# Performance work log

Hardware: AMD Instinct MI355X
Metric: run time of the kernel (lower is better)

Reference implementation:

```python
import jax, jax.numpy as jnp
import numpy as np

EPS = 1e-6      # torch F.pairwise_distance default eps (added to the difference)
MARGIN = 0.5


def setup_inputs() -> dict:
    key = jax.random.key(0)
    k1, k2 = jax.random.split(key)
    batch = jax.random.normal(k1, (8192, 1024), dtype=jnp.float32)
    positive = jax.random.normal(k2, (1024,), dtype=jnp.float32)
    return {"batch": batch, "positive": positive}


def _loss(batch, positive):
    n, d = batch.shape
    # torch pairwise_distance(x, y) = ||x - y + eps||_2, so
    # ||a - b + eps||^2 = ||a||^2 + ||b||^2 - 2 a.b + 2*eps*(sum(a) - sum(b)) + d*eps^2
    sq = jnp.sum(batch * batch, axis=-1)                 # [n]
    dots = batch @ batch.T                               # [n, n] GEMM
    sums = jnp.sum(batch, axis=-1)                       # [n]
    d2 = (sq[:, None] + sq[None, :] - 2.0 * dots
          + 2.0 * EPS * (sums[:, None] - sums[None, :]) + d * EPS * EPS)
    # exclude self (the python loop concatenates batch[:i], batch[i+1:])
    neg_inf = jnp.asarray(-jnp.inf, d2.dtype)
    d2_masked = jnp.where(jnp.eye(n, dtype=bool), neg_inf, d2)
    max_neg = jnp.sqrt(jnp.maximum(jnp.max(d2_masked, axis=-1), 0.0))  # [n]
    # distance anchor -> positive (with torch eps convention)
    diff = batch - positive[None, :] + EPS
    pos_dist = jnp.sqrt(jnp.sum(diff * diff, axis=-1))   # [n]
    losses = jax.nn.relu(pos_dist - max_neg + MARGIN)    # [n]
    # anchors exactly equal to the positive are skipped in the original loop
    valid = ~jnp.all(batch == positive[None, :], axis=-1)
    cnt = jnp.sum(valid.astype(losses.dtype))
    return jnp.sum(jnp.where(valid, losses, 0.0)) / cnt


def reference(batch, positive):
    return _loss(batch, positive)
```

## Files before the change

### kernel.cpp

```cpp
#include <hip/hip_runtime.h>
#include <hip/hip_bf16.h>


#define NROWS 8192
#define DIM   1024
#define BTM   256
#define BTN   128
#define BK    32
#define NKT   (DIM / BK)
#define NUNITS 1056

constexpr float EPS = 1e-6f;
constexpr float MARGIN = 0.5f;

typedef __attribute__((ext_vector_type(8))) short short8;
typedef __attribute__((ext_vector_type(4))) float f32x4;

__device__ __forceinline__ unsigned short f2bf_rne(float f) {
    unsigned u = __float_as_uint(f);
    u += 0x7fffu + ((u >> 16) & 1u);
    return (unsigned short)(u >> 16);
}

__global__ void prep_kernel(const float* __restrict__ X, const float* __restrict__ P,
                            unsigned short* __restrict__ Xb,
                            float* __restrict__ cj, float* __restrict__ basei,
                            float* __restrict__ posd, int* __restrict__ valid)
{
    const int tid  = threadIdx.x;
    const int w    = tid >> 6;
    const int lane = tid & 63;
    const int row  = blockIdx.x * 4 + w;
    const float* xr = X + (size_t)row * DIM;

    float sq = 0.f, sm = 0.f, pd = 0.f;
    bool eq = true;
    #pragma unroll
    for (int it = 0; it < 4; ++it) {
        const int idx = it * 256 + lane * 4;
        const float4 x = *(const float4*)(xr + idx);
        const float4 p = *(const float4*)(P + idx);
        sq += x.x*x.x + x.y*x.y + x.z*x.z + x.w*x.w;
        sm += x.x + x.y + x.z + x.w;
        const float d0 = x.x - p.x + EPS, d1 = x.y - p.y + EPS;
        const float d2 = x.z - p.z + EPS, d3 = x.w - p.w + EPS;
        pd += d0*d0 + d1*d1 + d2*d2 + d3*d3;
        eq = eq && (x.x == p.x) && (x.y == p.y) && (x.z == p.z) && (x.w == p.w);
        ushort4 b;
        b.x = f2bf_rne(x.x); b.y = f2bf_rne(x.y); b.z = f2bf_rne(x.z); b.w = f2bf_rne(x.w);
        *(ushort4*)(Xb + (size_t)row * DIM + idx) = b;
    }
    #pragma unroll
    for (int off = 32; off >= 1; off >>= 1) {
        sq += __shfl_xor(sq, off);
        sm += __shfl_xor(sm, off);
        pd += __shfl_xor(pd, off);
    }
    const bool alleq = __all(eq);
    if (lane == 0) {
        cj[row]    = sq - 2.f * EPS * sm;
        basei[row] = sq + 2.f * EPS * sm + (float)DIM * EPS * EPS;
        posd[row]  = sqrtf(pd);
        valid[row] = alleq ? 0 : 1;
    }
}

__global__ __launch_bounds__(512, 4) void gemm_max_kernel(
        const unsigned short* __restrict__ Xb,
        const float* __restrict__ cj,
        float* __restrict__ partmax)
{
    __shared__ alignas(16) unsigned short lds[3][1536 * 8];

    const int tid  = threadIdx.x;
    const int lane = tid & 63;
    const int wid  = tid >> 6;
    const int wm   = wid >> 1;
    const int wn   = wid & 1;
    const int l15  = lane & 15;
    const int lk   = lane >> 4;
    const int cx   = lk ^ ((l15 >> 1) & 3);

    {
        const unsigned h = ((unsigned)blockIdx.x * 2654435761u) >> 29;
        for (unsigned i = 0; i < h; ++i) __builtin_amdgcn_s_sleep(2);
    }

    const int t0 = (blockIdx.x & 7) * (NUNITS / 8) + (blockIdx.x >> 3);
    int bm = (int)(32.5f - sqrtf(1056.25f - (float)t0));
    if (bm < 0) bm = 0;
    if (bm > 31) bm = 31;
    while (bm > 0 && 65 * bm - bm * bm > t0) --bm;
    while (65 * (bm + 1) - (bm + 1) * (bm + 1) <= t0) ++bm;
    const int bn = 2 * bm + (t0 - (65 * bm - bm * bm));
    const int Mbase = bm * BTM, Nbase = bn * BTN;

    f32x4 acc[4][4];
    #pragma unroll
    for (int m = 0; m < 4; ++m)
        #pragma unroll
        for (int n = 0; n < 4; ++n)
            acc[m][n] = (f32x4){0.f, 0.f, 0.f, 0.f};

    const int qa0 = tid,        ra0 = qa0 >> 2, ca0 = (qa0 & 3) ^ ((qa0 >> 3) & 3);
    const int qa1 = 512 + tid,  ra1 = qa1 >> 2, ca1 = (qa1 & 3) ^ ((qa1 >> 3) & 3);
    const unsigned short* sA0 = Xb + (size_t)(Mbase + ra0) * DIM + ca0 * 8;
    const unsigned short* sA1 = Xb + (size_t)(Mbase + ra1) * DIM + ca1 * 8;
    const unsigned short* sB0 = Xb + (size_t)(Nbase + ra0) * DIM + ca0 * 8;

    #define STAGE_K(SB, KT) do {                                                              \
        __builtin_amdgcn_global_load_lds((const __attribute__((address_space(1))) void*)(sA0 + (KT) * BK), \
                (__attribute__((address_space(3))) void*)(&lds[SB][(wid * 64) * 8]), 16, 0, 0); \
        __builtin_amdgcn_global_load_lds((const __attribute__((address_space(1))) void*)(sA1 + (KT) * BK), \
                (__attribute__((address_space(3))) void*)(&lds[SB][(512 + wid * 64) * 8]), 16, 0, 0); \
        __builtin_amdgcn_global_load_lds((const __attribute__((address_space(1))) void*)(sB0 + (KT) * BK), \
                (__attribute__((address_space(3))) void*)(&lds[SB][(1024 + wid * 64) * 8]), 16, 0, 0); \
    } while (0)

    const int aoff = ((wm * 64 + l15) * 4 + cx) * 8;
    const int boff = 1024 * 8 + ((wn * 64 + l15) * 4 + cx) * 8;

    #define KT_BODY(RB, SB, KTS, VMC, DOSTAGE) do {                                           \
        asm volatile("s_waitcnt vmcnt(" #VMC ")" ::: "memory");                               \
        __builtin_amdgcn_s_barrier();                                                         \
        __builtin_amdgcn_sched_barrier(0);                                                    \
        if (DOSTAGE) STAGE_K(SB, KTS);                                                        \
        short8 af[4], bf[4];                                                                  \
        _Pragma("unroll")                                                                     \
        for (int mt = 0; mt < 4; ++mt)                                                        \
            af[mt] = *(const short8*)(&lds[RB][0] + aoff + mt * 512);                         \
        _Pragma("unroll")                                                                     \
        for (int nt = 0; nt < 4; ++nt)                                                        \
            bf[nt] = *(const short8*)(&lds[RB][0] + boff + nt * 512);                         \
        __builtin_amdgcn_s_setprio(1);                                                        \
        _Pragma("unroll")                                                                     \
        for (int mt = 0; mt < 4; ++mt)                                                        \
            _Pragma("unroll")                                                                 \
            for (int nt = 0; nt < 4; ++nt)                                                    \
                acc[mt][nt] = __builtin_amdgcn_mfma_f32_16x16x32_bf16(af[mt], bf[nt], acc[mt][nt], 0, 0, 0); \
        __builtin_amdgcn_s_setprio(0);                                                        \
    } while (0)

    STAGE_K(0, 0);
    STAGE_K(1, 1);

    for (int ktb = 0; ktb < 30; ktb += 3) {
        KT_BODY(0, 2, ktb + 2, 3, true);
        KT_BODY(1, 0, ktb + 3, 3, true);
        KT_BODY(2, 1, ktb + 4, 3, true);
    }
    KT_BODY(0, 2, 0, 3, false);
    KT_BODY(1, 2, 0, 0, false);
    #undef KT_BODY
    #undef STAGE_K

    float* scratchf = (float*)&lds[0][0];
    float cv[4];
    #pragma unroll
    for (int n = 0; n < 4; ++n)
        cv[n] = cj[Nbase + wn * 64 + n * 16 + l15];

    float vt[4];
    #pragma unroll
    for (int n = 0; n < 4; ++n) vt[n] = -__builtin_inff();

    #pragma unroll
    for (int m = 0; m < 4; ++m) {
        #pragma unroll
        for (int r = 0; r < 4; ++r) {
            const int lrow = wm * 64 + m * 16 + lk * 4 + r;
            const int grow = Mbase + lrow;
            const float ci = cj[grow];
            float rv = -__builtin_inff();
            #pragma unroll
            for (int n = 0; n < 4; ++n) {
                const float dot2 = 2.f * acc[m][n][r];
                const bool dg = (grow == Nbase + wn * 64 + n * 16 + l15);
                float vr = cv[n] - dot2;
                float vc = ci - dot2;
                if (dg) { vr = -__builtin_inff(); vc = -__builtin_inff(); }
                rv = fmaxf(rv, vr);
                vt[n] = fmaxf(vt[n], vc);
            }
            #pragma unroll
            for (int off = 8; off >= 1; off >>= 1)
                rv = fmaxf(rv, __shfl_xor(rv, off));
            if (l15 == 0) scratchf[wn * 256 + lrow] = rv;
        }
    }
    #pragma unroll
    for (int n = 0; n < 4; ++n) {
        vt[n] = fmaxf(vt[n], __shfl_xor(vt[n], 16));
        vt[n] = fmaxf(vt[n], __shfl_xor(vt[n], 32));
        if (lk == 0) scratchf[512 + wm * 128 + wn * 64 + n * 16 + l15] = vt[n];
    }
    __syncthreads();

    if (tid < BTM) {
        partmax[(size_t)bn * NROWS + Mbase + tid] = fmaxf(scratchf[tid], scratchf[256 + tid]);
    } else if (tid < BTM + BTN) {
        const int c = tid - BTM;
        const float v = fmaxf(fmaxf(scratchf[512 + c], scratchf[640 + c]),
                              fmaxf(scratchf[768 + c], scratchf[896 + c]));
        partmax[(size_t)(64 + bm) * NROWS + Nbase + c] = v;
    }
}

__global__ void finalize1_kernel(const float* __restrict__ partmax,
                                 const float* __restrict__ basei,
                                 const float* __restrict__ posd,
                                 const int* __restrict__ valid,
                                 float* __restrict__ partials)
{
    const int tid = threadIdx.x;
    const int a   = blockIdx.x;
    const int row = a * 256 + tid;
    float m = -__builtin_inff();
    for (int bn = 2 * a; bn < 64; ++bn)
        m = fmaxf(m, partmax[(size_t)bn * NROWS + row]);
    for (int bm2 = 0; bm2 <= a; ++bm2)
        m = fmaxf(m, partmax[(size_t)(64 + bm2) * NROWS + row]);
    const float d2 = m + basei[row];
    const float mn = sqrtf(fmaxf(d2, 0.f));
    float loss = fmaxf(posd[row] - mn + MARGIN, 0.f);
    float cnt = 1.f;
    if (!valid[row]) { loss = 0.f; cnt = 0.f; }
    #pragma unroll
    for (int off = 32; off >= 1; off >>= 1) {
        loss += __shfl_xor(loss, off);
        cnt  += __shfl_xor(cnt, off);
    }
    __shared__ float sl[4], sc[4];
    const int w = tid >> 6, lane = tid & 63;
    if (lane == 0) { sl[w] = loss; sc[w] = cnt; }
    __syncthreads();
    if (tid == 0) {
        partials[blockIdx.x * 2]     = sl[0] + sl[1] + sl[2] + sl[3];
        partials[blockIdx.x * 2 + 1] = sc[0] + sc[1] + sc[2] + sc[3];
    }
}

__global__ void finalize2_kernel(const float* __restrict__ partials, float* __restrict__ out)
{
    const int tid = threadIdx.x;
    float l = 0.f, c = 0.f;
    if (tid < 32) { l = partials[tid * 2]; c = partials[tid * 2 + 1]; }
    #pragma unroll
    for (int off = 32; off >= 1; off >>= 1) {
        l += __shfl_xor(l, off);
        c += __shfl_xor(c, off);
    }
    if (tid == 0) out[0] = l / c;
}

extern "C" void kernel_launch(void* const* d_in, const int* in_sizes, int n_in,
                              void* d_out, int out_size, void* d_ws, size_t ws_size,
                              hipStream_t stream)
{
    const float* X = (const float*)d_in[0];
    const float* P = (const float*)d_in[1];
    float* out = (float*)d_out;
    char* ws = (char*)d_ws;

    unsigned short* Xb = (unsigned short*)ws;
    size_t off = (size_t)NROWS * DIM * sizeof(unsigned short);
    float* cj    = (float*)(ws + off);  off += (size_t)NROWS * 4;
    float* basei = (float*)(ws + off);  off += (size_t)NROWS * 4;
    float* posd  = (float*)(ws + off);  off += (size_t)NROWS * 4;
    int*   valid = (int*)(ws + off);    off += (size_t)NROWS * 4;
    float* partmax = (float*)(ws + off); off += (size_t)96 * NROWS * 4;
    float* partials = (float*)(ws + off);

    prep_kernel<<<NROWS / 4, 256, 0, stream>>>(X, P, Xb, cj, basei, posd, valid);
    gemm_max_kernel<<<NUNITS, 512, 0, stream>>>(Xb, cj, partmax);
    finalize1_kernel<<<NROWS / 256, 256, 0, stream>>>(partmax, basei, posd, valid, partials);
    finalize2_kernel<<<1, 64, 0, stream>>>(partials, out);
}
```

Baseline: 112.9 us.

## Fuse row-max reduction and loss finalize into GEMM via atomics and last-block

Replaces the per-tile partial-max buffer and two finalize kernels with order-preserving unsigned atomicMax into a per-row max array. A global counter marks the last-finishing GEMM block, which then computes the loss and mean directly. This removes two kernel launches and the write and read of the large partial-max buffer. In exchange it adds contention on the row-max atomics and leaves the final reduction serialized in a single block.

```diff
diff --git a/kernel.cpp b/kernel.cpp
--- a/kernel.cpp
+++ b/kernel.cpp
@@ -22,16 +22,27 @@
     return (unsigned short)(u >> 16);
 }
 
+__device__ __forceinline__ unsigned fkey(float f) {
+    unsigned b = __float_as_uint(f);
+    return (b & 0x80000000u) ? ~b : (b | 0x80000000u);
+}
+__device__ __forceinline__ float finv(unsigned k) {
+    return __uint_as_float((k & 0x80000000u) ? (k & 0x7FFFFFFFu) : ~k);
+}
+
 __global__ void prep_kernel(const float* __restrict__ X, const float* __restrict__ P,
                             unsigned short* __restrict__ Xb,
                             float* __restrict__ cj, float* __restrict__ basei,
-                            float* __restrict__ posd, int* __restrict__ valid)
+                            float* __restrict__ posd, int* __restrict__ valid,
+                            unsigned* __restrict__ rowmax_u, unsigned* __restrict__ counter)
 {
     const int tid  = threadIdx.x;
     const int w    = tid >> 6;
     const int lane = tid & 63;
     const int row  = blockIdx.x * 4 + w;
     const float* xr = X + (size_t)row * DIM;
+
+    if (blockIdx.x == 0 && tid == 0) *counter = 0u;
 
     float sq = 0.f, sm = 0.f, pd = 0.f;
     bool eq = true;
@@ -58,19 +69,27 @@
     }
     const bool alleq = __all(eq);
     if (lane == 0) {
-        cj[row]    = sq - 2.f * EPS * sm;
-        basei[row] = sq + 2.f * EPS * sm + (float)DIM * EPS * EPS;
-        posd[row]  = sqrtf(pd);
-        valid[row] = alleq ? 0 : 1;
+        cj[row]       = sq - 2.f * EPS * sm;
+        basei[row]    = sq + 2.f * EPS * sm + (float)DIM * EPS * EPS;
+        posd[row]     = sqrtf(pd);
+        valid[row]    = alleq ? 0 : 1;
+        rowmax_u[row] = 0u;
     }
 }
 
 __global__ __launch_bounds__(512, 4) void gemm_max_kernel(
         const unsigned short* __restrict__ Xb,
         const float* __restrict__ cj,
-        float* __restrict__ partmax)
+        const float* __restrict__ basei,
+        const float* __restrict__ posd,
+        const int* __restrict__ valid,
+        unsigned* __restrict__ rowmax_u,
+        unsigned* __restrict__ counter,
+        float* __restrict__ out)
 {
     __shared__ alignas(16) unsigned short lds[3][1536 * 8];
+    __shared__ int lastflag;
+    __shared__ float sl[8], sc[8];
 
     const int tid  = threadIdx.x;
     const int lane = tid & 63;
@@ -197,60 +216,47 @@
     __syncthreads();
 
     if (tid < BTM) {
-        partmax[(size_t)bn * NROWS + Mbase + tid] = fmaxf(scratchf[tid], scratchf[256 + tid]);
+        const float v = fmaxf(scratchf[tid], scratchf[256 + tid]);
+        atomicMax(&rowmax_u[Mbase + tid], fkey(v));
     } else if (tid < BTM + BTN) {
         const int c = tid - BTM;
         const float v = fmaxf(fmaxf(scratchf[512 + c], scratchf[640 + c]),
                               fmaxf(scratchf[768 + c], scratchf[896 + c]));
-        partmax[(size_t)(64 + bm) * NROWS + Nbase + c] = v;
-    }
-}
-
-__global__ void finalize1_kernel(const float* __restrict__ partmax,
-                                 const float* __restrict__ basei,
-                                 const float* __restrict__ posd,
-                                 const int* __restrict__ valid,
-                                 float* __restrict__ partials)
-{
-    const int tid = threadIdx.x;
-    const int a   = blockIdx.x;
-    const int row = a * 256 + tid;
-    float m = -__builtin_inff();
-    for (int bn = 2 * a; bn < 64; ++bn)
-        m = fmaxf(m, partmax[(size_t)bn * NROWS + row]);
-    for (int bm2 = 0; bm2 <= a; ++bm2)
-        m = fmaxf(m, partmax[(size_t)(64 + bm2) * NROWS + row]);
-    const float d2 = m + basei[row];
-    const float mn = sqrtf(fmaxf(d2, 0.f));
-    float loss = fmaxf(posd[row] - mn + MARGIN, 0.f);
-    float cnt = 1.f;
-    if (!valid[row]) { loss = 0.f; cnt = 0.f; }
+        atomicMax(&rowmax_u[Nbase + c], fkey(v));
+    }
+
+    __threadfence();
+    __syncthreads();
+    if (tid == 0) {
+        const unsigned old = atomicAdd(counter, 1u);
+        lastflag = (old == NUNITS - 1) ? 1 : 0;
+    }
+    __syncthreads();
+    if (!lastflag) return;
+    __threadfence();
+
+    float lsum = 0.f, csum = 0.f;
+    for (int r = tid; r < NROWS; r += 512) {
+        const unsigned k = atomicMax(&rowmax_u[r], 0u);
+        const float m = finv(k);
+        const float d2 = m + basei[r];
+        const float mn = sqrtf(fmaxf(d2, 0.f));
+        const float loss = fmaxf(posd[r] - mn + MARGIN, 0.f);
+        if (valid[r]) { lsum += loss; csum += 1.f; }
+    }
     #pragma unroll
     for (int off = 32; off >= 1; off >>= 1) {
-        loss += __shfl_xor(loss, off);
-        cnt  += __shfl_xor(cnt, off);
-    }
-    __shared__ float sl[4], sc[4];
-    const int w = tid >> 6, lane = tid & 63;
-    if (lane == 0) { sl[w] = loss; sc[w] = cnt; }
+        lsum += __shfl_xor(lsum, off);
+        csum += __shfl_xor(csum, off);
+    }
+    if (lane == 0) { sl[wid] = lsum; sc[wid] = csum; }
     __syncthreads();
     if (tid == 0) {
-        partials[blockIdx.x * 2]     = sl[0] + sl[1] + sl[2] + sl[3];
-        partials[blockIdx.x * 2 + 1] = sc[0] + sc[1] + sc[2] + sc[3];
-    }
-}
-
-__global__ void finalize2_kernel(const float* __restrict__ partials, float* __restrict__ out)
-{
-    const int tid = threadIdx.x;
-    float l = 0.f, c = 0.f;
-    if (tid < 32) { l = partials[tid * 2]; c = partials[tid * 2 + 1]; }
-    #pragma unroll
-    for (int off = 32; off >= 1; off >>= 1) {
-        l += __shfl_xor(l, off);
-        c += __shfl_xor(c, off);
-    }
-    if (tid == 0) out[0] = l / c;
+        float L = 0.f, C = 0.f;
+        #pragma unroll
+        for (int i = 0; i < 8; ++i) { L += sl[i]; C += sc[i]; }
+        out[0] = L / C;
+    }
 }
 
 extern "C" void kernel_launch(void* const* d_in, const int* in_sizes, int n_in,
@@ -268,11 +274,11 @@
     float* basei = (float*)(ws + off);  off += (size_t)NROWS * 4;
     float* posd  = (float*)(ws + off);  off += (size_t)NROWS * 4;
     int*   valid = (int*)(ws + off);    off += (size_t)NROWS * 4;
-    float* partmax = (float*)(ws + off); off += (size_t)96 * NROWS * 4;
-    float* partials = (float*)(ws + off);
-
-    prep_kernel<<<NROWS / 4, 256, 0, stream>>>(X, P, Xb, cj, basei, posd, valid);
-    gemm_max_kernel<<<NUNITS, 512, 0, stream>>>(Xb, cj, partmax);
-    finalize1_kernel<<<NROWS / 256, 256, 0, stream>>>(partmax, basei, posd, valid, partials);
-    finalize2_kernel<<<1, 64, 0, stream>>>(partials, out);
-}
+    unsigned* rowmax_u = (unsigned*)(ws + off); off += (size_t)NROWS * 4;
+    unsigned* counter  = (unsigned*)(ws + off); off += 256;
+
+    prep_kernel<<<NROWS / 4, 256, 0, stream>>>(X, P, Xb, cj, basei, posd, valid,
+                                               rowmax_u, counter);
+    gemm_max_kernel<<<NUNITS, 512, 0, stream>>>(Xb, cj, basei, posd, valid,
+                                                rowmax_u, counter, out);
+}
```

New measurement: 279.2 us. 2.47x slower.
